# Kernel optimization log

Measured on AMD Instinct MI355X. Metric: run time of the kernel, lower is better.

The kernel has to match this reference:

```python
import jax, jax.numpy as jnp
import numpy as np

BOUND = 3.0
MIN_BIN_W = 1e-3   # min_bin_width
MIN_BIN_H = 1e-3   # min_bin_height
MIN_DERIV = 1e-3   # min_derivative
MIN_LAMBDA = 0.025
EPS = 1e-6


def _knots(frac, min_size, left, right):
    # frac: [D, K] normalized (softmax) bin fractions -> (bin sizes [D,K], knot positions [D,K+1])
    K = frac.shape[-1]
    sizes = min_size + (1.0 - min_size * K) * frac
    cum = jnp.cumsum(sizes, axis=-1)
    cum = jnp.concatenate([jnp.zeros_like(cum[..., :1]), cum], axis=-1)
    cum = (right - left) * cum + left
    cum = cum.at[..., 0].set(left)
    cum = cum.at[..., -1].set(right)
    sizes = cum[..., 1:] - cum[..., :-1]
    return sizes, cum


def _spline_fwd(x, uw, uh, ud, ul, bound=BOUND):
    # x: [B, D]; uw/uh/ul: [D, K]; ud: [D, K-1]
    B, D = x.shape
    K = uw.shape[-1]
    w = jax.nn.softmax(uw, axis=-1)
    h = jax.nn.softmax(uh, axis=-1)
    d = MIN_DERIV + jax.nn.softplus(ud)
    lam = MIN_LAMBDA + (1.0 - 2.0 * MIN_LAMBDA) * jax.nn.sigmoid(ul)

    left, right = -bound, bound
    widths, cumwidths = _knots(w, MIN_BIN_W, left, right)
    heights, cumheights = _knots(h, MIN_BIN_H, left, right)
    ones = jnp.ones_like(d[..., :1])
    derivs = jnp.concatenate([ones, d, ones], axis=-1)  # [D, K+1]; identity slope at the tails

    inside = (x >= left) & (x <= right)
    xc = jnp.clip(x, left, right)  # keep spline branch NaN-free for outside points

    # bucketize: index of bin containing each input, per dimension  -> [B, D]
    bin_idx = jnp.sum(xc[..., None] >= (cumwidths + EPS)[None], axis=-1) - 1
    bin_idx = jnp.clip(bin_idx, 0, K - 1)

    def sel(t):
        # gather per-(sample, dim) bin parameter: t [D, K or K+1] -> [B, D]
        tb = jnp.broadcast_to(t[None], (B,) + t.shape)
        return jnp.take_along_axis(tb, bin_idx[..., None], axis=-1)[..., 0]

    iw, icw = sel(widths), sel(cumwidths)
    ih, ich = sel(heights), sel(cumheights)
    idelta = sel(heights / widths)
    d0, d1 = sel(derivs), sel(derivs[..., 1:])
    il = sel(lam)

    # monotonic *linear* rational spline (Dolatabadi et al.), forward direction
    wa = 1.0
    wb = jnp.sqrt(d0 / d1) * wa
    wc = (il * wa * d0 + (1.0 - il) * wb * d1) / idelta
    ya = ich
    yb = ih + ich
    yc = ((1.0 - il) * wa * ya + il * wb * yb) / ((1.0 - il) * wa + il * wb)

    theta = (xc - icw) / iw
    lo = theta <= il
    num = jnp.where(lo,
                    wa * ya * (il - theta) + wc * yc * theta,
                    wc * yc * (1.0 - theta) + wb * yb * (theta - il))
    den = jnp.where(lo,
                    wa * (il - theta) + wc * theta,
                    wc * (1.0 - theta) + wb * (theta - il))
    dnum = jnp.where(lo,
                     wa * wc * il * (yc - ya),
                     wb * wc * (1.0 - il) * (yb - yc)) / iw

    u = jnp.where(inside, num / den, x)                      # identity outside the box
    logabsdet = jnp.where(inside, jnp.log(dnum) - 2.0 * jnp.log(jnp.abs(den)), 0.0)
    return u, jnp.sum(logabsdet, axis=1)


def setup_inputs() -> dict:
    B, D, K = 32768, 256, 32
    key = jax.random.key(0)
    k1, k2, k3, k4, k5 = jax.random.split(key, 5)
    return {
        "x": jax.random.normal(k1, (B, D), jnp.float32),
        "uw": jax.random.normal(k2, (D, K), jnp.float32),
        "uh": jax.random.normal(k3, (D, K), jnp.float32),
        "ud": jax.random.normal(k4, (D, K - 1), jnp.float32),
        "ul": jax.random.uniform(k5, (D, K), jnp.float32),
    }


def reference(x, uw, uh, ud, ul):
    # f: data x -> latent u, plus log|det J| summed over feature dim
    return _spline_fwd(x, uw, uh, ud, ul)
```

## Files before the change

### kernel.cpp

```cpp
#include <hip/hip_runtime.h>
#include <hip/hip_fp16.h>
#include <math.h>
#include <stdint.h>

#define D_DIM 256
#define K_BINS 32
#define NCELL 512
#define NENT 34
#define ENT_DW 8
#define ENT_STRIDE 276
#define LIC_STRIDE 35
#define LUT_BSTRIDE 516
#define SLICE 16

static constexpr float BOUND = 3.0f;
static constexpr float MIN_BIN_W = 1e-3f;
static constexpr float MIN_DERIV = 1e-3f;
static constexpr float MIN_LAMBDA = 0.025f;
static constexpr float EPS_ = 1e-6f;
static constexpr float CELL_W = 6.0f / NCELL;
static constexpr float CELL_S = NCELL / 6.0f;
static constexpr float LN2_ = 0.69314718055994531f;

__device__ __forceinline__ float softplusf_(float x) {
  return fmaxf(x, 0.0f) + log1pf(expf(-fabsf(x)));
}

__device__ __forceinline__ float pack2h_as_f32(float a, float b) {
  __half2 h = __halves2half2(__float2half_rn(a), __float2half_rn(b));
  union { __half2 h; uint32_t u; } c;
  c.h = h;
  return __uint_as_float(c.u);
}

__device__ __forceinline__ float2 unpack2h_from_f32(float v) {
  union { uint32_t u; __half2 h; } c;
  c.u = __float_as_uint(v);
  return make_float2(__low2float(c.h), __high2float(c.h));
}

__global__ void spline_precompute(const float* __restrict__ uw,
                                  const float* __restrict__ uh,
                                  const float* __restrict__ ud,
                                  const float* __restrict__ ul,
                                  float* __restrict__ tblg,
                                  float* __restrict__ licg,
                                  uint8_t* __restrict__ lutg) {
  __shared__ float cw_lds[8][32];

  int tid = threadIdx.x;
  int k = tid & 31;
  int dsub = tid >> 5;
  int d = blockIdx.x * 8 + dsub;

  float uwv = uw[d * K_BINS + k];
  float uhv = uh[d * K_BINS + k];
  float ulv = ul[d * K_BINS + k];
  float udv = (k < K_BINS - 1) ? ud[d * (K_BINS - 1) + k] : 0.0f;

  float wm = uwv, hm = uhv;
  for (int o = 16; o; o >>= 1) {
    wm = fmaxf(wm, __shfl_xor(wm, o, 32));
    hm = fmaxf(hm, __shfl_xor(hm, o, 32));
  }
  float ew = expf(uwv - wm), eh = expf(uhv - hm);
  float ws = ew, hs = eh;
  for (int o = 16; o; o >>= 1) {
    ws += __shfl_xor(ws, o, 32);
    hs += __shfl_xor(hs, o, 32);
  }
  const float kfac = 1.0f - MIN_BIN_W * (float)K_BINS;
  float sw = MIN_BIN_W + kfac * (ew / ws);
  float sh = MIN_BIN_W + kfac * (eh / hs);

  float cws = sw, chs = sh;
  for (int o = 1; o < 32; o <<= 1) {
    float tw = __shfl_up(cws, o, 32);
    float th = __shfl_up(chs, o, 32);
    if (k >= o) { cws += tw; chs += th; }
  }
  const float scale = 2.0f * BOUND;
  float raw_w = scale * cws - BOUND;
  float raw_h = scale * chs - BOUND;
  float upw = __shfl_up(raw_w, 1, 32);
  float uph = __shfl_up(raw_h, 1, 32);
  float cw_lo = (k == 0) ? -BOUND : upw;
  float ch_lo = (k == 0) ? -BOUND : uph;
  float cw_hi = (k == K_BINS - 1) ? BOUND : raw_w;
  float ch_hi = (k == K_BINS - 1) ? BOUND : raw_h;

  float iw = cw_hi - cw_lo;
  float ih = ch_hi - ch_lo;

  float dk = MIN_DERIV + softplusf_(udv);
  float dprev = __shfl_up(dk, 1, 32);
  float d1 = (k == K_BINS - 1) ? 1.0f : dk;
  float d0 = (k == 0) ? 1.0f : dprev;

  float sg = 1.0f / (1.0f + expf(-ulv));
  float lam = MIN_LAMBDA + (1.0f - 2.0f * MIN_LAMBDA) * sg;

  float wb = sqrtf(d0 / d1);
  float delta = ih / iw;
  float wc = (lam * d0 + (1.0f - lam) * wb * d1) / delta;
  float denom = (1.0f - lam) + lam * wb;
  float dyc = lam * wb * ih / denom;
  float dyb = ih - dyc;
  float ya = ch_lo;
  float inv_iw = 1.0f / iw;
  float yc = ya + dyc;

  float* e = tblg + (size_t)(d * NENT + k) * ENT_DW;
  e[0] = cw_lo;
  e[1] = inv_iw;
  e[2] = lam;
  e[3] = wc;
  e[4] = wb;
  e[5] = yc;
  e[6] = pack2h_as_f32(dyc, dyb);
  e[7] = pack2h_as_f32(log2f(wc * lam * dyc * inv_iw),
                       log2f(wc * wb * (1.0f - lam) * dyb * inv_iw));
  licg[d * NENT + k] = cw_lo + EPS_;
  cw_lds[dsub][k] = cw_lo;

  if (tid < 8 * 2 * ENT_DW) {
    int dim = tid >> 4;
    int r = tid & 15;
    int ks = 32 + (r >> 3);
    int f = r & 7;
    int dd = blockIdx.x * 8 + dim;
    tblg[((size_t)(dd * NENT + ks)) * ENT_DW + f] = (f == 0) ? 1e30f : 0.0f;
  }
  if (tid < 16) {
    int dim = tid >> 1;
    int ks = 32 + (tid & 1);
    licg[(blockIdx.x * 8 + dim) * NENT + ks] = 1e30f;
  }
  __syncthreads();

  for (int rep = 0; rep < 16; ++rep) {
    int idx = rep * 256 + tid;
    int dim = idx >> 9;
    int c = idx & (NCELL - 1);
    float L = fmaf((float)c, CELL_W, -BOUND) - 1e-5f;
    int j = 0;
#pragma unroll
    for (int st = 16; st >= 1; st >>= 1) {
      float cv = cw_lds[dim][j + st];
      j = (L >= cv + EPS_) ? j + st : j;
    }
    lutg[(blockIdx.x * 8 + dim) * NCELL + c] = (uint8_t)j;
  }
}

__global__ __launch_bounds__(512, 8) void spline_main(
    const float* __restrict__ x,
    const float* __restrict__ tblg,
    const float* __restrict__ licg,
    const uint8_t* __restrict__ lutg,
    float* __restrict__ uout,
    float* __restrict__ part,
    int B) {
  __shared__ float lent[SLICE * ENT_STRIDE];
  __shared__ float lic[SLICE * LIC_STRIDE];
  __shared__ uint8_t lutb[SLICE * LUT_BSTRIDE];

  int tid = threadIdx.x;
  int slice = blockIdx.x & 15;
  int group = blockIdx.x >> 4;
  int d0 = slice * SLICE;

  const float* esrc = tblg + (size_t)d0 * NENT * ENT_DW;
  for (int i = tid; i < SLICE * NENT * ENT_DW; i += 512) {
    int dim = i / (NENT * ENT_DW);
    int rem = i - dim * (NENT * ENT_DW);
    lent[dim * ENT_STRIDE + rem] = esrc[i];
  }
  const float* lsrc = licg + (size_t)d0 * NENT;
  for (int i = tid; i < SLICE * NENT; i += 512) {
    int dim = i / NENT;
    int kk = i - dim * NENT;
    lic[dim * LIC_STRIDE + kk] = lsrc[i];
  }
  const uint32_t* lut32 = (const uint32_t*)(lutg + (size_t)d0 * NCELL);
  uint32_t* lutb32 = (uint32_t*)lutb;
  for (int i = tid; i < SLICE * (NCELL / 4); i += 512) {
    int dim = i >> 7;
    int w = i & 127;
    lutb32[dim * (LUT_BSTRIDE / 4) + w] = lut32[i];
  }
  __syncthreads();

  int lane = tid & 63;
  int wid = tid >> 6;
  int r4 = lane >> 4;
  int dsl = lane & 15;

  int row0 = group * 32 + wid * 4 + r4;
  size_t base = (size_t)row0 * D_DIM + d0 + dsl;
  const int entb = dsl * ENT_STRIDE;
  const int licb = dsl * LIC_STRIDE;
  const int lutbase = dsl * LUT_BSTRIDE;
  float* parts = part + (size_t)slice * B;

  int niter = B >> 11;
  for (int it = 0; it < niter; ++it) {
    int row = row0 + (it << 11);
    size_t gidx = base + ((size_t)it << 11) * D_DIM;

    float xv = x[gidx];
    float xc = fminf(fmaxf(xv, -BOUND), BOUND);
    bool inside = fabsf(xv) <= BOUND;

    float cf = fmaf(xc, CELL_S, (float)(NCELL / 2));
    int c = (int)cf;
    c = min(c, NCELL - 1);
    int ilut = (int)lutb[lutbase + c];

    float c1 = lic[licb + ilut + 1];
    float c2 = lic[licb + ilut + 2];
    int idx = ilut + (xc >= c1 ? 1 : 0) + (xc >= c2 ? 1 : 0);

    int eb = entb + idx * ENT_DW;
    float4 A = *reinterpret_cast<const float4*>(&lent[eb]);
    float4 Bv = *reinterpret_cast<const float4*>(&lent[eb + 4]);

    float icw = A.x, inv_iw = A.y, il = A.z, wcv = A.w;
    float wbv = Bv.x, yc = Bv.y;
    float2 dd = unpack2h_from_f32(Bv.z);
    float2 LL = unpack2h_from_f32(Bv.w);

    float theta = (xc - icw) * inv_iw;
    bool lo = theta <= il;
    float t1 = il - theta;
    float t3 = 1.0f - theta;

    float den = lo ? fmaf(wcv, theta, t1)
                   : fmaf(wcv, t3, -(wbv * t1));
    float sfac = lo ? dd.x : (wbv * dd.y);
    float Ls = lo ? LL.x : LL.y;

    float r = __builtin_amdgcn_rcpf(den);
    float uu = fmaf(-t1 * sfac, r, yc);
    float lad2 = fmaf(-2.0f, __builtin_amdgcn_logf(den), Ls);

    uout[gidx] = inside ? uu : xv;
    float ls = inside ? lad2 : 0.0f;

    ls += __shfl_down(ls, 8, 16);
    ls += __shfl_down(ls, 4, 16);
    ls += __shfl_down(ls, 2, 16);
    ls += __shfl_down(ls, 1, 16);
    if (dsl == 0) parts[row] = ls;
  }
}

__global__ void spline_reduce(const float* __restrict__ part,
                              float* __restrict__ ldout, int B) {
  int row = blockIdx.x * 256 + threadIdx.x;
  if (row >= B) return;
  float s = 0.0f;
#pragma unroll
  for (int sl = 0; sl < D_DIM / SLICE; ++sl) s += part[(size_t)sl * B + row];
  ldout[row] = s * LN2_;
}

extern "C" void kernel_launch(void* const* d_in, const int* in_sizes, int n_in,
                              void* d_out, int out_size, void* d_ws, size_t ws_size,
                              hipStream_t stream) {
  const float* x  = (const float*)d_in[0];
  const float* uw = (const float*)d_in[1];
  const float* uh = (const float*)d_in[2];
  const float* ud = (const float*)d_in[3];
  const float* ul = (const float*)d_in[4];

  int B = in_sizes[0] / D_DIM;

  float* out = (float*)d_out;
  float* uout = out;
  float* ldout = out + (size_t)B * D_DIM;

  char* ws = (char*)d_ws;
  float* tblg = (float*)ws;
  float* licg = (float*)(ws + 278528);
  uint8_t* lutg = (uint8_t*)(ws + 278528 + 34816);
  float* part = (float*)(ws + 278528 + 34816 + 131072);

  spline_precompute<<<32, 256, 0, stream>>>(uw, uh, ud, ul, tblg, licg, lutg);
  spline_main<<<1024, 512, 0, stream>>>(x, tblg, licg, lutg, uout, part, B);
  spline_reduce<<<(B + 255) / 256, 256, 0, stream>>>(part, ldout, B);
}
```

Before: 34.05 us.

## Fuse spline parameter precompute into main kernel, building tables in LDS

Removes the separate precompute kernel. Each main-kernel block now computes the softmax, knot, derivative and lambda tables for its own 16 dimensions directly into shared memory, instead of loading them from a global workspace. The bin lookup table is filled by ranges: each bin lane finds its first cell and writes its index up to the next bin's start. This drops one launch and the global write/read of the tables, at the cost of redundant per-block transcendental work and a serial per-lane fill loop before the first sync.

```diff
diff --git a/kernel.cpp b/kernel.cpp
--- a/kernel.cpp
+++ b/kernel.cpp
@@ -6,9 +6,8 @@
 #define D_DIM 256
 #define K_BINS 32
 #define NCELL 512
-#define NENT 34
 #define ENT_DW 8
-#define ENT_STRIDE 276
+#define ENT_STRIDE 260
 #define LIC_STRIDE 35
 #define LUT_BSTRIDE 516
 #define SLICE 16
@@ -39,125 +38,12 @@
   return make_float2(__low2float(c.h), __high2float(c.h));
 }
 
-__global__ void spline_precompute(const float* __restrict__ uw,
-                                  const float* __restrict__ uh,
-                                  const float* __restrict__ ud,
-                                  const float* __restrict__ ul,
-                                  float* __restrict__ tblg,
-                                  float* __restrict__ licg,
-                                  uint8_t* __restrict__ lutg) {
-  __shared__ float cw_lds[8][32];
-
-  int tid = threadIdx.x;
-  int k = tid & 31;
-  int dsub = tid >> 5;
-  int d = blockIdx.x * 8 + dsub;
-
-  float uwv = uw[d * K_BINS + k];
-  float uhv = uh[d * K_BINS + k];
-  float ulv = ul[d * K_BINS + k];
-  float udv = (k < K_BINS - 1) ? ud[d * (K_BINS - 1) + k] : 0.0f;
-
-  float wm = uwv, hm = uhv;
-  for (int o = 16; o; o >>= 1) {
-    wm = fmaxf(wm, __shfl_xor(wm, o, 32));
-    hm = fmaxf(hm, __shfl_xor(hm, o, 32));
-  }
-  float ew = expf(uwv - wm), eh = expf(uhv - hm);
-  float ws = ew, hs = eh;
-  for (int o = 16; o; o >>= 1) {
-    ws += __shfl_xor(ws, o, 32);
-    hs += __shfl_xor(hs, o, 32);
-  }
-  const float kfac = 1.0f - MIN_BIN_W * (float)K_BINS;
-  float sw = MIN_BIN_W + kfac * (ew / ws);
-  float sh = MIN_BIN_W + kfac * (eh / hs);
-
-  float cws = sw, chs = sh;
-  for (int o = 1; o < 32; o <<= 1) {
-    float tw = __shfl_up(cws, o, 32);
-    float th = __shfl_up(chs, o, 32);
-    if (k >= o) { cws += tw; chs += th; }
-  }
-  const float scale = 2.0f * BOUND;
-  float raw_w = scale * cws - BOUND;
-  float raw_h = scale * chs - BOUND;
-  float upw = __shfl_up(raw_w, 1, 32);
-  float uph = __shfl_up(raw_h, 1, 32);
-  float cw_lo = (k == 0) ? -BOUND : upw;
-  float ch_lo = (k == 0) ? -BOUND : uph;
-  float cw_hi = (k == K_BINS - 1) ? BOUND : raw_w;
-  float ch_hi = (k == K_BINS - 1) ? BOUND : raw_h;
-
-  float iw = cw_hi - cw_lo;
-  float ih = ch_hi - ch_lo;
-
-  float dk = MIN_DERIV + softplusf_(udv);
-  float dprev = __shfl_up(dk, 1, 32);
-  float d1 = (k == K_BINS - 1) ? 1.0f : dk;
-  float d0 = (k == 0) ? 1.0f : dprev;
-
-  float sg = 1.0f / (1.0f + expf(-ulv));
-  float lam = MIN_LAMBDA + (1.0f - 2.0f * MIN_LAMBDA) * sg;
-
-  float wb = sqrtf(d0 / d1);
-  float delta = ih / iw;
-  float wc = (lam * d0 + (1.0f - lam) * wb * d1) / delta;
-  float denom = (1.0f - lam) + lam * wb;
-  float dyc = lam * wb * ih / denom;
-  float dyb = ih - dyc;
-  float ya = ch_lo;
-  float inv_iw = 1.0f / iw;
-  float yc = ya + dyc;
-
-  float* e = tblg + (size_t)(d * NENT + k) * ENT_DW;
-  e[0] = cw_lo;
-  e[1] = inv_iw;
-  e[2] = lam;
-  e[3] = wc;
-  e[4] = wb;
-  e[5] = yc;
-  e[6] = pack2h_as_f32(dyc, dyb);
-  e[7] = pack2h_as_f32(log2f(wc * lam * dyc * inv_iw),
-                       log2f(wc * wb * (1.0f - lam) * dyb * inv_iw));
-  licg[d * NENT + k] = cw_lo + EPS_;
-  cw_lds[dsub][k] = cw_lo;
-
-  if (tid < 8 * 2 * ENT_DW) {
-    int dim = tid >> 4;
-    int r = tid & 15;
-    int ks = 32 + (r >> 3);
-    int f = r & 7;
-    int dd = blockIdx.x * 8 + dim;
-    tblg[((size_t)(dd * NENT + ks)) * ENT_DW + f] = (f == 0) ? 1e30f : 0.0f;
-  }
-  if (tid < 16) {
-    int dim = tid >> 1;
-    int ks = 32 + (tid & 1);
-    licg[(blockIdx.x * 8 + dim) * NENT + ks] = 1e30f;
-  }
-  __syncthreads();
-
-  for (int rep = 0; rep < 16; ++rep) {
-    int idx = rep * 256 + tid;
-    int dim = idx >> 9;
-    int c = idx & (NCELL - 1);
-    float L = fmaf((float)c, CELL_W, -BOUND) - 1e-5f;
-    int j = 0;
-#pragma unroll
-    for (int st = 16; st >= 1; st >>= 1) {
-      float cv = cw_lds[dim][j + st];
-      j = (L >= cv + EPS_) ? j + st : j;
-    }
-    lutg[(blockIdx.x * 8 + dim) * NCELL + c] = (uint8_t)j;
-  }
-}
-
-__global__ __launch_bounds__(512, 8) void spline_main(
+__global__ __launch_bounds__(512, 8) void spline_fused(
     const float* __restrict__ x,
-    const float* __restrict__ tblg,
-    const float* __restrict__ licg,
-    const uint8_t* __restrict__ lutg,
+    const float* __restrict__ uw,
+    const float* __restrict__ uh,
+    const float* __restrict__ ud,
+    const float* __restrict__ ul,
     float* __restrict__ uout,
     float* __restrict__ part,
     int B) {
@@ -170,24 +56,95 @@
   int group = blockIdx.x >> 4;
   int d0 = slice * SLICE;
 
-  const float* esrc = tblg + (size_t)d0 * NENT * ENT_DW;
-  for (int i = tid; i < SLICE * NENT * ENT_DW; i += 512) {
-    int dim = i / (NENT * ENT_DW);
-    int rem = i - dim * (NENT * ENT_DW);
-    lent[dim * ENT_STRIDE + rem] = esrc[i];
-  }
-  const float* lsrc = licg + (size_t)d0 * NENT;
-  for (int i = tid; i < SLICE * NENT; i += 512) {
-    int dim = i / NENT;
-    int kk = i - dim * NENT;
-    lic[dim * LIC_STRIDE + kk] = lsrc[i];
-  }
-  const uint32_t* lut32 = (const uint32_t*)(lutg + (size_t)d0 * NCELL);
-  uint32_t* lutb32 = (uint32_t*)lutb;
-  for (int i = tid; i < SLICE * (NCELL / 4); i += 512) {
-    int dim = i >> 7;
-    int w = i & 127;
-    lutb32[dim * (LUT_BSTRIDE / 4) + w] = lut32[i];
+  {
+    int k = tid & 31;
+    int dim = tid >> 5;
+    int d = d0 + dim;
+
+    float uwv = uw[d * K_BINS + k];
+    float uhv = uh[d * K_BINS + k];
+    float ulv = ul[d * K_BINS + k];
+    float udv = (k < K_BINS - 1) ? ud[d * (K_BINS - 1) + k] : 0.0f;
+
+    float wm = uwv, hm = uhv;
+    for (int o = 16; o; o >>= 1) {
+      wm = fmaxf(wm, __shfl_xor(wm, o, 32));
+      hm = fmaxf(hm, __shfl_xor(hm, o, 32));
+    }
+    float ew = expf(uwv - wm), eh = expf(uhv - hm);
+    float ws = ew, hs = eh;
+    for (int o = 16; o; o >>= 1) {
+      ws += __shfl_xor(ws, o, 32);
+      hs += __shfl_xor(hs, o, 32);
+    }
+    const float kfac = 1.0f - MIN_BIN_W * (float)K_BINS;
+    float sw = MIN_BIN_W + kfac * (ew / ws);
+    float sh = MIN_BIN_W + kfac * (eh / hs);
+
+    float cws = sw, chs = sh;
+    for (int o = 1; o < 32; o <<= 1) {
+      float tw = __shfl_up(cws, o, 32);
+      float th = __shfl_up(chs, o, 32);
+      if (k >= o) { cws += tw; chs += th; }
+    }
+    const float scale = 2.0f * BOUND;
+    float raw_w = scale * cws - BOUND;
+    float raw_h = scale * chs - BOUND;
+    float upw = __shfl_up(raw_w, 1, 32);
+    float uph = __shfl_up(raw_h, 1, 32);
+    float cw_lo = (k == 0) ? -BOUND : upw;
+    float ch_lo = (k == 0) ? -BOUND : uph;
+    float cw_hi = (k == K_BINS - 1) ? BOUND : raw_w;
+    float ch_hi = (k == K_BINS - 1) ? BOUND : raw_h;
+
+    float iw = cw_hi - cw_lo;
+    float ih = ch_hi - ch_lo;
+
+    float dk = MIN_DERIV + softplusf_(udv);
+    float dprev = __shfl_up(dk, 1, 32);
+    float d1 = (k == K_BINS - 1) ? 1.0f : dk;
+    float dd0 = (k == 0) ? 1.0f : dprev;
+
+    float sg = 1.0f / (1.0f + expf(-ulv));
+    float lam = MIN_LAMBDA + (1.0f - 2.0f * MIN_LAMBDA) * sg;
+
+    float wb = sqrtf(dd0 / d1);
+    float delta = ih / iw;
+    float wc = (lam * dd0 + (1.0f - lam) * wb * d1) / delta;
+    float denom = (1.0f - lam) + lam * wb;
+    float dyc = lam * wb * ih / denom;
+    float dyb = ih - dyc;
+    float ya = ch_lo;
+    float inv_iw = 1.0f / iw;
+    float yc = ya + dyc;
+
+    float* e = &lent[dim * ENT_STRIDE + k * ENT_DW];
+    e[0] = cw_lo;
+    e[1] = inv_iw;
+    e[2] = lam;
+    e[3] = wc;
+    e[4] = wb;
+    e[5] = yc;
+    e[6] = pack2h_as_f32(dyc, dyb);
+    e[7] = pack2h_as_f32(log2f(wc * lam * dyc * inv_iw),
+                         log2f(wc * wb * (1.0f - lam) * dyb * inv_iw));
+
+    float t = cw_lo + EPS_;
+    lic[dim * LIC_STRIDE + k] = t;
+    if (k < 2) lic[dim * LIC_STRIDE + 32 + k] = 1e30f;
+
+    int c0 = 0;
+    if (k > 0) {
+      float q = (t + BOUND + 1e-5f) * CELL_S;
+      c0 = (int)ceilf(q);
+      if (c0 < 0) c0 = 0;
+      if (c0 > NCELL) c0 = NCELL;
+      while (c0 < NCELL && (fmaf((float)c0, CELL_W, -BOUND) - 1e-5f) < t) ++c0;
+      while (c0 > 0 && (fmaf((float)(c0 - 1), CELL_W, -BOUND) - 1e-5f) >= t) --c0;
+    }
+    int c1 = __shfl_down(c0, 1, 32);
+    if (k == K_BINS - 1) c1 = NCELL;
+    for (int c = c0; c < c1; ++c) lutb[dim * LUT_BSTRIDE + c] = (uint8_t)k;
   }
   __syncthreads();
 
@@ -280,13 +237,8 @@
   float* uout = out;
   float* ldout = out + (size_t)B * D_DIM;
 
-  char* ws = (char*)d_ws;
-  float* tblg = (float*)ws;
-  float* licg = (float*)(ws + 278528);
-  uint8_t* lutg = (uint8_t*)(ws + 278528 + 34816);
-  float* part = (float*)(ws + 278528 + 34816 + 131072);
-
-  spline_precompute<<<32, 256, 0, stream>>>(uw, uh, ud, ul, tblg, licg, lutg);
-  spline_main<<<1024, 512, 0, stream>>>(x, tblg, licg, lutg, uout, part, B);
-  spline_reduce<<<(B + 255) / 256, 256, 0, stream>>>(part, ldout, B);
-}
+  float* partw = (float*)d_ws;
+
+  spline_fused<<<1024, 512, 0, stream>>>(x, uw, uh, ud, ul, uout, partw, B);
+  spline_reduce<<<(B + 255) / 256, 256, 0, stream>>>(partw, ldout, B);
+}
```

Result: no change. 34.21 us (+0.5%).
